# Kernel tuning notes

Hardware: AMD Instinct MI355X
Metric: run time of the kernel (lower is better)

The kernel has to match this reference:

```python
import jax, jax.numpy as jnp
import numpy as np

N_NODES = 50000
N_EDGES = 800000
ALPHA = 0.2  # LeakyReLU negative slope


def setup_inputs() -> dict:
    key = jax.random.key(0)
    ks = jax.random.split(key, 12)
    F_IN, H, D, NOUT = 256, 8, 64, 64

    def xavier(k, shape):
        fan_in, fan_out = shape[-2], shape[-1]
        limit = np.sqrt(6.0 / (fan_in + fan_out)).astype(np.float32)
        return jax.random.uniform(k, shape, jnp.float32, -limit, limit)

    x = jax.random.normal(ks[0], (N_NODES, F_IN), jnp.float32)
    edge_src = jnp.sort(jax.random.randint(ks[1], (N_EDGES,), 0, N_NODES, jnp.int32))
    edge_dst = jax.random.randint(ks[2], (N_EDGES,), 0, N_NODES, jnp.int32)
    return {
        'x': x,
        'edge_src': edge_src,
        'edge_dst': edge_dst,
        'W1': xavier(ks[3], (H, F_IN, D)),
        'a_src1': xavier(ks[4], (H, D, 1))[..., 0],
        'a_dst1': xavier(ks[5], (H, D, 1))[..., 0],
        'W2': xavier(ks[6], (H, H * D, D)),
        'a_src2': xavier(ks[7], (H, D, 1))[..., 0],
        'a_dst2': xavier(ks[8], (H, D, 1))[..., 0],
        'lin_W': xavier(ks[9], (H * D, NOUT)),
        'lin_b': jnp.zeros((NOUT,), jnp.float32),
    }


def _gat_layer(x, W, a_s, a_d, src, dst, n_nodes):
    # W: [H, F, D]; x: [N, F]
    Wh = jnp.einsum('nf,hfd->nhd', x, W)                  # [N, H, D]
    f1 = jnp.einsum('nhd,hd->nh', Wh, a_s)                # score from row node
    f2 = jnp.einsum('nhd,hd->nh', Wh, a_d)                # score from col node
    e = f1[src] + f2[dst]                                 # [E, H]
    e = jnp.where(e > 0, e, ALPHA * e)                    # LeakyReLU
    # sparse softmax over neighbors of each row (dim=1 in torch.sparse.softmax)
    m = jax.ops.segment_max(e, src, num_segments=n_nodes)
    m = jnp.where(jnp.isfinite(m), m, 0.0)                # guard empty segments
    p = jnp.exp(e - m[src])
    s = jax.ops.segment_sum(p, src, num_segments=n_nodes)
    att = p / jnp.maximum(s[src], 1e-16)                  # [E, H]
    # spmm: per-head to cap the [E, D] message buffer
    H = W.shape[0]
    outs = []
    for h in range(H):
        msg = att[:, h:h + 1] * Wh[dst, h, :]             # [E, D]
        outs.append(jax.ops.segment_sum(msg, src, num_segments=n_nodes))
    hp = jnp.stack(outs, axis=1)                          # [N, H, D]
    hp = jax.nn.elu(hp)
    return hp.reshape(n_nodes, -1)                        # concat heads -> [N, H*D]


def reference(x, edge_src, edge_dst, W1, a_src1, a_dst1, W2, a_src2, a_dst2, lin_W, lin_b):
    n = x.shape[0]
    h = _gat_layer(x, W1, a_src1, a_dst1, edge_src, edge_dst, n)
    h = _gat_layer(h, W2, a_src2, a_dst2, edge_src, edge_dst, n)
    return h @ lin_W + lin_b                              # [N, nout]
```

## Files before the change

### kernel.cpp

```cpp
#include <hip/hip_runtime.h>
#include <hip/hip_bf16.h>
#include <math.h>

#define ALPHA 0.2f
#define N_NODES 50000
#define N_EDGES 800000
#define HEADS 8
#define DH 64
#define HD 512
#define DCAP 128

typedef __attribute__((ext_vector_type(8))) short short8v;
typedef __attribute__((ext_vector_type(4))) float float4v;

__device__ __forceinline__ unsigned short f2bf(float f) {
    unsigned int u = __float_as_uint(f);
    unsigned int r = (u + 0x7fffu + ((u >> 16) & 1u)) >> 16;
    return (unsigned short)r;
}
__device__ __forceinline__ float bf2f(unsigned short h) {
    return __uint_as_float(((unsigned int)h) << 16);
}

__device__ __forceinline__ void gl_lds16(const unsigned short* g, unsigned short* l) {
    __builtin_amdgcn_global_load_lds(
        (const __attribute__((address_space(1))) unsigned int*)(g),
        (__attribute__((address_space(3))) unsigned int*)(l),
        16, 0, 0);
}

__global__ void build_rowptr(const int* __restrict__ src, int E, int n_nodes,
                             int* __restrict__ row_ptr) {
    int n = blockIdx.x * blockDim.x + threadIdx.x;
    if (n > n_nodes) return;
    int lo = 0, hi = E;
    while (lo < hi) {
        int mid = (lo + hi) >> 1;
        if (src[mid] < n) lo = mid + 1; else hi = mid;
    }
    row_ptr[n] = lo;
}

__global__ __launch_bounds__(256) void cast_bf16(
    const float* __restrict__ in, unsigned short* __restrict__ out, int total8) {
    int i = blockIdx.x * 256 + threadIdx.x;
    if (i >= total8) return;
    const float4* p = reinterpret_cast<const float4*>(in + (size_t)i * 8);
    float4 v0 = p[0], v1 = p[1];
    float vv[8] = {v0.x, v0.y, v0.z, v0.w, v1.x, v1.y, v1.z, v1.w};
    short8v o;
    #pragma unroll
    for (int q = 0; q < 8; ++q) o[q] = (short)f2bf(vv[q]);
    *reinterpret_cast<short8v*>(out + (size_t)i * 8) = o;
}

__global__ void transpose_w_bf(const float* __restrict__ in,
                               unsigned short* __restrict__ outB,
                               int F, int total) {
    int idx = blockIdx.x * 256 + threadIdx.x;
    if (idx >= total) return;
    int d = idx & 63;
    int f = (idx >> 6) % F;
    int h = idx / (F << 6);
    outB[(size_t)((h << 6) + d) * F + f] = f2bf(in[idx]);
}

__global__ __launch_bounds__(512) void gemm_bf16_fused(
    const unsigned short* __restrict__ A,
    const unsigned short* __restrict__ B,
    const float* __restrict__ bias,
    float* __restrict__ C, unsigned short* __restrict__ Cbf,
    const float* __restrict__ a_s, const float* __restrict__ a_d,
    float* __restrict__ f1out, float* __restrict__ f2out,
    int M, int K, int N)
{
    __shared__ unsigned short As[128][64];
    __shared__ unsigned short Bs[256][64];

    const int tid = threadIdx.x;
    const int bm = blockIdx.x * 128;
    const int bn = blockIdx.y * 256;
    const int wid = tid >> 6;
    const int lane = tid & 63;

    const int wr = (wid >> 2) * 64;
    const int wc = (wid & 3) * 64;
    const int fr = lane & 15;
    const int fks = (lane >> 4) * 8;

    const int a_r = lane >> 3;
    const int a_c = 8 * ((lane & 7) ^ a_r);

    float4v acc[4][4];
    #pragma unroll
    for (int m = 0; m < 4; ++m)
        #pragma unroll
        for (int n = 0; n < 4; ++n)
            acc[m][n] = (float4v){0.f, 0.f, 0.f, 0.f};

    for (int k0 = 0; k0 < K; k0 += 64) {
        #pragma unroll
        for (int i = 0; i < 2; ++i) {
            int g = wid * 2 + i;
            int row = bm + g * 8 + a_r; if (row >= M) row = M - 1;
            gl_lds16(&A[(size_t)row * K + k0 + a_c], &As[g * 8][0]);
        }
        #pragma unroll
        for (int i = 0; i < 4; ++i) {
            int g = wid * 4 + i;
            int row = bn + g * 8 + a_r; if (row >= N) row = N - 1;
            gl_lds16(&B[(size_t)row * K + k0 + a_c], &Bs[g * 8][0]);
        }
        __syncthreads();

        #pragma unroll
        for (int ks = 0; ks < 2; ++ks) {
            const int fko = ks * 32 + fks;
            short8v aF[4], bF[4];
            #pragma unroll
            for (int m = 0; m < 4; ++m) {
                int rr = wr + m * 16 + fr;
                aF[m] = *reinterpret_cast<const short8v*>(&As[rr][fko ^ ((rr & 7) * 8)]);
            }
            #pragma unroll
            for (int n = 0; n < 4; ++n) {
                int cc = wc + n * 16 + fr;
                bF[n] = *reinterpret_cast<const short8v*>(&Bs[cc][fko ^ ((cc & 7) * 8)]);
            }
            #pragma unroll
            for (int m = 0; m < 4; ++m)
                #pragma unroll
                for (int n = 0; n < 4; ++n)
                    acc[m][n] = __builtin_amdgcn_mfma_f32_16x16x32_bf16(aF[m], bF[n], acc[m][n], 0, 0, 0);
        }
        __syncthreads();
    }

    if (f1out) {
        const int head = (bn + wc) >> 6;
        float asv[4], adv[4];
        #pragma unroll
        for (int n = 0; n < 4; ++n) {
            asv[n] = a_s[bn + wc + n * 16 + fr];
            adv[n] = a_d[bn + wc + n * 16 + fr];
        }
        #pragma unroll
        for (int m = 0; m < 4; ++m) {
            #pragma unroll
            for (int r = 0; r < 4; ++r) {
                float ps = 0.f, pd = 0.f;
                #pragma unroll
                for (int n = 0; n < 4; ++n) {
                    ps += acc[m][n][r] * asv[n];
                    pd += acc[m][n][r] * adv[n];
                }
                #pragma unroll
                for (int mk = 1; mk <= 8; mk <<= 1) {
                    ps += __shfl_xor(ps, mk);
                    pd += __shfl_xor(pd, mk);
                }
                int row = bm + wr + m * 16 + (lane >> 4) * 4 + r;
                if (fr == 0 && row < M) {
                    f1out[(size_t)row * HEADS + head] = ps;
                    f2out[(size_t)row * HEADS + head] = pd;
                }
            }
        }
    }

    #pragma unroll
    for (int m = 0; m < 4; ++m) {
        int row0 = bm + wr + m * 16 + (lane >> 4) * 4;
        #pragma unroll
        for (int n = 0; n < 4; ++n) {
            int col = bn + wc + n * 16 + fr;
            if (col >= N) continue;
            float b = bias ? bias[col] : 0.f;
            #pragma unroll
            for (int r = 0; r < 4; ++r) {
                int row = row0 + r;
                if (row < M) {
                    if (Cbf) Cbf[(size_t)row * N + col] = f2bf(acc[m][n][r]);
                    else     C[(size_t)row * N + col] = acc[m][n][r] + b;
                }
            }
        }
    }
}

__global__ __launch_bounds__(256) void gat_node_wave(
    const unsigned short* __restrict__ Wh, const float* __restrict__ f1,
    const float* __restrict__ f2, const int* __restrict__ row_ptr,
    const int* __restrict__ dst, unsigned short* __restrict__ out, int n_nodes)
{
    __shared__ float s_p[4][DCAP][HEADS];
    __shared__ int   s_dst[4][DCAP];

    const int wv = threadIdx.x >> 6;
    const int lane = threadIdx.x & 63;
    const int n = blockIdx.x * 4 + wv;
    if (n >= n_nodes) return;

    const int lo = row_ptr[n], hi = row_ptr[n + 1];
    const int deg = hi - lo;

    const int h  = lane & 7;
    const int j8 = lane >> 3;
    const int hl = lane >> 3;
    const int dg = (lane & 7) * 8;
    const size_t base = (size_t)hl * DH + dg;

    const float f1h = f1[(size_t)n * HEADS + h];

    float m = -INFINITY;
    for (int b0 = 0; b0 < deg; b0 += 8) {
        int j = b0 + j8;
        float e = -INFINITY;
        if (j < deg) {
            int dn = dst[lo + j];
            e = f1h + f2[(size_t)dn * HEADS + h];
            e = e > 0.f ? e : ALPHA * e;
        }
        m = fmaxf(m, e);
    }
    #pragma unroll
    for (int mk = 8; mk <= 32; mk <<= 1) m = fmaxf(m, __shfl_xor(m, mk));

    float ssum = 0.f;
    float acc[8] = {0.f, 0.f, 0.f, 0.f, 0.f, 0.f, 0.f, 0.f};

    for (int c0 = 0; c0 < deg; c0 += DCAP) {
        int cn = min(DCAP, deg - c0);
        for (int b0 = 0; b0 < cn; b0 += 8) {
            int j = b0 + j8;
            float p = 0.f;
            if (j < cn) {
                int dn = dst[lo + c0 + j];
                float e = f1h + f2[(size_t)dn * HEADS + h];
                e = e > 0.f ? e : ALPHA * e;
                p = __expf(e - m);
                s_p[wv][j][h] = p;
                if (h == 0) s_dst[wv][j] = dn;
            }
            ssum += p;
        }
        asm volatile("s_waitcnt lgkmcnt(0)" ::: "memory");

        int j = 0;
        for (; j + 4 <= cn; j += 4) {
            int dn0 = s_dst[wv][j + 0];
            int dn1 = s_dst[wv][j + 1];
            int dn2 = s_dst[wv][j + 2];
            int dn3 = s_dst[wv][j + 3];
            float p0 = s_p[wv][j + 0][hl];
            float p1 = s_p[wv][j + 1][hl];
            float p2 = s_p[wv][j + 2][hl];
            float p3 = s_p[wv][j + 3][hl];
            uint4 u0 = *reinterpret_cast<const uint4*>(&Wh[(size_t)dn0 * HD + base]);
            uint4 u1 = *reinterpret_cast<const uint4*>(&Wh[(size_t)dn1 * HD + base]);
            uint4 u2 = *reinterpret_cast<const uint4*>(&Wh[(size_t)dn2 * HD + base]);
            uint4 u3 = *reinterpret_cast<const uint4*>(&Wh[(size_t)dn3 * HD + base]);
            unsigned int w0[4] = {u0.x, u0.y, u0.z, u0.w};
            unsigned int w1[4] = {u1.x, u1.y, u1.z, u1.w};
            unsigned int w2[4] = {u2.x, u2.y, u2.z, u2.w};
            unsigned int w3[4] = {u3.x, u3.y, u3.z, u3.w};
            #pragma unroll
            for (int q = 0; q < 4; ++q) {
                acc[2 * q]     += p0 * __uint_as_float(w0[q] << 16);
                acc[2 * q + 1] += p0 * __uint_as_float(w0[q] & 0xffff0000u);
                acc[2 * q]     += p1 * __uint_as_float(w1[q] << 16);
                acc[2 * q + 1] += p1 * __uint_as_float(w1[q] & 0xffff0000u);
                acc[2 * q]     += p2 * __uint_as_float(w2[q] << 16);
                acc[2 * q + 1] += p2 * __uint_as_float(w2[q] & 0xffff0000u);
                acc[2 * q]     += p3 * __uint_as_float(w3[q] << 16);
                acc[2 * q + 1] += p3 * __uint_as_float(w3[q] & 0xffff0000u);
            }
        }
        for (; j < cn; ++j) {
            int dn = s_dst[wv][j];
            float p = s_p[wv][j][hl];
            uint4 u = *reinterpret_cast<const uint4*>(&Wh[(size_t)dn * HD + base]);
            unsigned int uu[4] = {u.x, u.y, u.z, u.w};
            #pragma unroll
            for (int q = 0; q < 4; ++q) {
                acc[2 * q]     += p * __uint_as_float(uu[q] << 16);
                acc[2 * q + 1] += p * __uint_as_float(uu[q] & 0xffff0000u);
            }
        }
        asm volatile("s_waitcnt lgkmcnt(0)" ::: "memory");
    }

    #pragma unroll
    for (int mk = 8; mk <= 32; mk <<= 1) ssum += __shfl_xor(ssum, mk);
    float inv = 1.f / fmaxf(ssum, 1e-16f);
    float invg = __shfl(inv, hl);

    short8v o8;
    #pragma unroll
    for (int q = 0; q < 8; ++q) {
        float v = acc[q] * invg;
        v = v > 0.f ? v : expm1f(v);
        o8[q] = (short)f2bf(v);
    }
    *reinterpret_cast<short8v*>(&out[(size_t)n * HD + hl * DH + dg]) = o8;
}

extern "C" void kernel_launch(void* const* d_in, const int* in_sizes, int n_in,
                              void* d_out, int out_size, void* d_ws, size_t ws_size,
                              hipStream_t stream) {
    const float* x      = (const float*)d_in[0];
    const int*   e_src  = (const int*)d_in[1];
    const int*   e_dst  = (const int*)d_in[2];
    const float* W1     = (const float*)d_in[3];
    const float* a_src1 = (const float*)d_in[4];
    const float* a_dst1 = (const float*)d_in[5];
    const float* W2     = (const float*)d_in[6];
    const float* a_src2 = (const float*)d_in[7];
    const float* a_dst2 = (const float*)d_in[8];
    const float* lin_W  = (const float*)d_in[9];
    const float* lin_b  = (const float*)d_in[10];
    float* outp = (float*)d_out;

    const size_t NHD = (size_t)N_NODES * HD;
    unsigned short* WhBf = (unsigned short*)d_ws;
    unsigned short* hBf  = WhBf + NHD;
    unsigned short* xBf  = hBf + NHD;
    float* f1    = (float*)(xBf + (size_t)N_NODES * 256);
    float* f2    = f1 + (size_t)N_NODES * HEADS;
    int* rowptr  = (int*)(f2 + (size_t)N_NODES * HEADS);
    unsigned short* BtW1  = (unsigned short*)(rowptr + N_NODES + 64);
    unsigned short* BtW2  = BtW1 + (size_t)HD * 256;
    unsigned short* BtLin = BtW2 + (size_t)HD * HD;

    build_rowptr<<<(N_NODES + 256) / 256, 256, 0, stream>>>(e_src, N_EDGES, N_NODES, rowptr);
    cast_bf16<<<(N_NODES * 256 / 8 + 255) / 256, 256, 0, stream>>>(x, xBf, N_NODES * 256 / 8);
    transpose_w_bf<<<(HEADS * 256 * DH + 255) / 256, 256, 0, stream>>>(W1, BtW1, 256, HEADS * 256 * DH);
    transpose_w_bf<<<(HEADS * HD * DH + 255) / 256, 256, 0, stream>>>(W2, BtW2, HD, HEADS * HD * DH);
    transpose_w_bf<<<(HD * 64 + 255) / 256, 256, 0, stream>>>(lin_W, BtLin, HD, HD * 64);

    const int nwb = (N_NODES + 3) / 4;
    dim3 g1((N_NODES + 127) / 128, HD / 256);

    gemm_bf16_fused<<<g1, 512, 0, stream>>>(xBf, BtW1, nullptr, nullptr, WhBf,
                                            a_src1, a_dst1, f1, f2, N_NODES, 256, HD);
    gat_node_wave<<<nwb, 256, 0, stream>>>(WhBf, f1, f2, rowptr, e_dst, hBf, N_NODES);

    gemm_bf16_fused<<<g1, 512, 0, stream>>>(hBf, BtW2, nullptr, nullptr, WhBf,
                                            a_src2, a_dst2, f1, f2, N_NODES, HD, HD);
    gat_node_wave<<<nwb, 256, 0, stream>>>(WhBf, f1, f2, rowptr, e_dst, hBf, N_NODES);

    dim3 g3((N_NODES + 127) / 128, 1);
    gemm_bf16_fused<<<g3, 512, 0, stream>>>(hBf, BtLin, lin_b, outp, nullptr,
                                            nullptr, nullptr, nullptr, nullptr, N_NODES, HD, 64);
}
```

Baseline: 397.8 us.

## Fuse preprocessing kernels into one launch and remap GEMM blocks per XCD

Merges the row-pointer build, the input cast and the three weight transposes into a single grid-stride preprocessing kernel, removing four kernel launches. The GEMM now uses a 1D grid and remaps block IDs so that consecutive tiles, including both column tiles of an M-row block, land on the same XCD, which is meant to improve L2 reuse of the A operand. The single preprocessing kernel has branchy mixed work per thread, and the remap must cover every tile exactly once.

```diff
diff --git a/kernel.cpp b/kernel.cpp
--- a/kernel.cpp
+++ b/kernel.cpp
@@ -29,40 +29,57 @@
         16, 0, 0);
 }
 
-__global__ void build_rowptr(const int* __restrict__ src, int E, int n_nodes,
-                             int* __restrict__ row_ptr) {
-    int n = blockIdx.x * blockDim.x + threadIdx.x;
-    if (n > n_nodes) return;
-    int lo = 0, hi = E;
-    while (lo < hi) {
-        int mid = (lo + hi) >> 1;
-        if (src[mid] < n) lo = mid + 1; else hi = mid;
-    }
-    row_ptr[n] = lo;
-}
-
-__global__ __launch_bounds__(256) void cast_bf16(
-    const float* __restrict__ in, unsigned short* __restrict__ out, int total8) {
-    int i = blockIdx.x * 256 + threadIdx.x;
-    if (i >= total8) return;
-    const float4* p = reinterpret_cast<const float4*>(in + (size_t)i * 8);
-    float4 v0 = p[0], v1 = p[1];
-    float vv[8] = {v0.x, v0.y, v0.z, v0.w, v1.x, v1.y, v1.z, v1.w};
-    short8v o;
-    #pragma unroll
-    for (int q = 0; q < 8; ++q) o[q] = (short)f2bf(vv[q]);
-    *reinterpret_cast<short8v*>(out + (size_t)i * 8) = o;
-}
-
-__global__ void transpose_w_bf(const float* __restrict__ in,
-                               unsigned short* __restrict__ outB,
-                               int F, int total) {
-    int idx = blockIdx.x * 256 + threadIdx.x;
-    if (idx >= total) return;
-    int d = idx & 63;
-    int f = (idx >> 6) % F;
-    int h = idx / (F << 6);
-    outB[(size_t)((h << 6) + d) * F + f] = f2bf(in[idx]);
+#define PPR0 50001
+#define PPR1 (PPR0 + 1600000)
+#define PPR2 (PPR1 + 131072)
+#define PPR3 (PPR2 + 262144)
+#define PPR4 (PPR3 + 32768)
+
+__global__ __launch_bounds__(256) void preproc(
+    const int* __restrict__ esrc, int* __restrict__ row_ptr,
+    const float* __restrict__ x, unsigned short* __restrict__ xBf,
+    const float* __restrict__ W1, unsigned short* __restrict__ BtW1,
+    const float* __restrict__ W2, unsigned short* __restrict__ BtW2,
+    const float* __restrict__ linW, unsigned short* __restrict__ BtLin)
+{
+    const int stride = gridDim.x * 256;
+    for (int i = blockIdx.x * 256 + threadIdx.x; i < PPR4; i += stride) {
+        if (i < PPR0) {
+            int n = i;
+            int lo = 0, hi = N_EDGES;
+            while (lo < hi) {
+                int mid = (lo + hi) >> 1;
+                if (esrc[mid] < n) lo = mid + 1; else hi = mid;
+            }
+            row_ptr[n] = lo;
+        } else if (i < PPR1) {
+            int idx = i - PPR0;
+            const float4* p = reinterpret_cast<const float4*>(x + (size_t)idx * 8);
+            float4 v0 = p[0], v1 = p[1];
+            float vv[8] = {v0.x, v0.y, v0.z, v0.w, v1.x, v1.y, v1.z, v1.w};
+            short8v o;
+            #pragma unroll
+            for (int q = 0; q < 8; ++q) o[q] = (short)f2bf(vv[q]);
+            *reinterpret_cast<short8v*>(xBf + (size_t)idx * 8) = o;
+        } else if (i < PPR2) {
+            int idx = i - PPR1;
+            int d = idx & 63;
+            int f = (idx >> 6) & 255;
+            int h = idx >> 14;
+            BtW1[(size_t)((h << 6) + d) * 256 + f] = f2bf(W1[idx]);
+        } else if (i < PPR3) {
+            int idx = i - PPR2;
+            int d = idx & 63;
+            int f = (idx >> 6) & 511;
+            int h = idx >> 15;
+            BtW2[(size_t)((h << 6) + d) * 512 + f] = f2bf(W2[idx]);
+        } else {
+            int idx = i - PPR3;
+            int o = idx & 63;
+            int k = idx >> 6;
+            BtLin[(size_t)o * 512 + k] = f2bf(linW[idx]);
+        }
+    }
 }
 
 __global__ __launch_bounds__(512) void gemm_bf16_fused(
@@ -72,14 +89,20 @@
     float* __restrict__ C, unsigned short* __restrict__ Cbf,
     const float* __restrict__ a_s, const float* __restrict__ a_d,
     float* __restrict__ f1out, float* __restrict__ f2out,
-    int M, int K, int N)
+    int M, int K, int N, int ncol)
 {
     __shared__ unsigned short As[128][64];
     __shared__ unsigned short Bs[256][64];
 
+    const int nwg = gridDim.x;
+    const int orig = blockIdx.x;
+    const int qq = nwg >> 3, rr8 = nwg & 7;
+    const int xcd = orig & 7, idx8 = orig >> 3;
+    const int wgid = (xcd < rr8 ? xcd * (qq + 1) : rr8 * (qq + 1) + (xcd - rr8) * qq) + idx8;
+    const int bm = (wgid / ncol) * 128;
+    const int bn = (wgid % ncol) * 256;
+
     const int tid = threadIdx.x;
-    const int bm = blockIdx.x * 128;
-    const int bn = blockIdx.y * 256;
     const int wid = tid >> 6;
     const int lane = tid & 63;
 
@@ -119,8 +142,8 @@
             short8v aF[4], bF[4];
             #pragma unroll
             for (int m = 0; m < 4; ++m) {
-                int rr = wr + m * 16 + fr;
-                aF[m] = *reinterpret_cast<const short8v*>(&As[rr][fko ^ ((rr & 7) * 8)]);
+                int rw = wr + m * 16 + fr;
+                aF[m] = *reinterpret_cast<const short8v*>(&As[rw][fko ^ ((rw & 7) * 8)]);
             }
             #pragma unroll
             for (int n = 0; n < 4; ++n) {
@@ -332,24 +355,19 @@
     unsigned short* BtW2  = BtW1 + (size_t)HD * 256;
     unsigned short* BtLin = BtW2 + (size_t)HD * HD;
 
-    build_rowptr<<<(N_NODES + 256) / 256, 256, 0, stream>>>(e_src, N_EDGES, N_NODES, rowptr);
-    cast_bf16<<<(N_NODES * 256 / 8 + 255) / 256, 256, 0, stream>>>(x, xBf, N_NODES * 256 / 8);
-    transpose_w_bf<<<(HEADS * 256 * DH + 255) / 256, 256, 0, stream>>>(W1, BtW1, 256, HEADS * 256 * DH);
-    transpose_w_bf<<<(HEADS * HD * DH + 255) / 256, 256, 0, stream>>>(W2, BtW2, HD, HEADS * HD * DH);
-    transpose_w_bf<<<(HD * 64 + 255) / 256, 256, 0, stream>>>(lin_W, BtLin, HD, HD * 64);
+    preproc<<<2048, 256, 0, stream>>>(e_src, rowptr, x, xBf, W1, BtW1, W2, BtW2, lin_W, BtLin);
 
     const int nwb = (N_NODES + 3) / 4;
-    dim3 g1((N_NODES + 127) / 128, HD / 256);
-
-    gemm_bf16_fused<<<g1, 512, 0, stream>>>(xBf, BtW1, nullptr, nullptr, WhBf,
-                                            a_src1, a_dst1, f1, f2, N_NODES, 256, HD);
+    const int nmb = (N_NODES + 127) / 128;
+
+    gemm_bf16_fused<<<nmb * 2, 512, 0, stream>>>(xBf, BtW1, nullptr, nullptr, WhBf,
+                                                 a_src1, a_dst1, f1, f2, N_NODES, 256, HD, 2);
     gat_node_wave<<<nwb, 256, 0, stream>>>(WhBf, f1, f2, rowptr, e_dst, hBf, N_NODES);
 
-    gemm_bf16_fused<<<g1, 512, 0, stream>>>(hBf, BtW2, nullptr, nullptr, WhBf,
-                                            a_src2, a_dst2, f1, f2, N_NODES, HD, HD);
+    gemm_bf16_fused<<<nmb * 2, 512, 0, stream>>>(hBf, BtW2, nullptr, nullptr, WhBf,
+                                                 a_src2, a_dst2, f1, f2, N_NODES, HD, HD, 2);
     gat_node_wave<<<nwb, 256, 0, stream>>>(WhBf, f1, f2, rowptr, e_dst, hBf, N_NODES);
 
-    dim3 g3((N_NODES + 127) / 128, 1);
-    gemm_bf16_fused<<<g3, 512, 0, stream>>>(hBf, BtLin, lin_b, outp, nullptr,
-                                            nullptr, nullptr, nullptr, nullptr, N_NODES, HD, 64);
-}
+    gemm_bf16_fused<<<nmb, 512, 0, stream>>>(hBf, BtLin, lin_b, outp, nullptr,
+                                             nullptr, nullptr, nullptr, nullptr, N_NODES, HD, 64, 1);
+}
```

After: 387.2 us. 1.03x faster.
